# Kernel tuning notes

Hardware: AMD Instinct MI355X
Metric: run time of the kernel (lower is better)

The kernel has to match this reference:

```python
import jax, jax.numpy as jnp
import numpy as np

VOC, D, CPR, RELS = 2048, 128, 128, 7
B, DEPTH = 512, 4  # complete binary trees: 2**DEPTH leaves per tree


def setup_inputs() -> dict:
    key = jax.random.key(0)
    ks = jax.random.split(key, 13)
    s = lambda k, shape, fan: jax.random.normal(k, shape, jnp.float32) / np.sqrt(fan)
    return {
        "leaf_ids": jax.random.randint(ks[0], (B, 2, 2 ** DEPTH), 0, VOC),
        "Wv": s(ks[1], (D, VOC), VOC), "bv": jnp.zeros((D,), jnp.float32),
        "Wcps": s(ks[2], (D, 2 * D), 2 * D), "bcps": jnp.zeros((D,), jnp.float32),
        "Wcpst": s(ks[3], (D, D * D), D * D), "bcpst": jnp.zeros((D,), jnp.float32),
        "Wcpr": s(ks[4], (CPR, 2 * D), 2 * D), "bcpr": jnp.zeros((CPR,), jnp.float32),
        "Wcprt": s(ks[5], (CPR, D * D), D * D), "bcprt": jnp.zeros((CPR,), jnp.float32),
        "Wsm": s(ks[6], (RELS, CPR), CPR), "bsm": jnp.zeros((RELS,), jnp.float32),
    }


def reference(leaf_ids, Wv, bv, Wcps, bcps, Wcpst, bcpst, Wcpr, bcpr, Wcprt, bcprt, Wsm, bsm):
    d = Wv.shape[0]
    # leaf embedding: voc(one_hot(idx)) == Wv[:, idx] + bv  -> [B, 2, L, d]
    h = jnp.take(Wv.T, leaf_ids, axis=0) + bv
    # batched level-by-level tree composition (complete binary trees)
    while h.shape[2] > 1:
        l, r = h[:, :, 0::2, :], h[:, :, 1::2, :]
        lin = jnp.concatenate([l, r], axis=-1) @ Wcps.T + bcps
        kron = (l[..., :, None] * r[..., None, :]).reshape(l.shape[:-1] + (d * d,))
        h = jnp.tanh(lin + kron @ Wcpst.T + bcpst)
    lc, rc = h[:, 0, 0, :], h[:, 1, 0, :]  # [B, d] each
    cpr = jnp.concatenate([lc, rc], axis=-1) @ Wcpr.T + bcpr
    kron = (lc[:, :, None] * rc[:, None, :]).reshape(lc.shape[0], d * d)
    act = jax.nn.leaky_relu(cpr + kron @ Wcprt.T + bcprt, 0.01)
    logits = act @ Wsm.T + bsm
    return jax.nn.log_softmax(logits, axis=-1)  # [B, RELS]
```

## Files before the change

### kernel.cpp

```cpp
#include <hip/hip_runtime.h>
#include <hip/hip_bf16.h>
#include <hip/hip_fp16.h>

#define DD    128
#define VOCAB 2048
#define NRELS 7
#define NWF   (130 * 16384)

typedef _Float16 f16;
typedef __attribute__((ext_vector_type(8))) _Float16 f16x8;
typedef __attribute__((ext_vector_type(4))) float    f32x4;

__device__ __forceinline__ float lde(const void* p, size_t i, int bf) {
    if (bf) return (float)((const __hip_bfloat16*)p)[i];
    return ((const float*)p)[i];
}

__global__ void detect_kernel(const unsigned short* __restrict__ wv, int* __restrict__ flag)
{
    if (threadIdx.x == 0 && blockIdx.x == 0) {
        int sane = 0;
        for (int i = 0; i < 64; ++i) {
            unsigned e = (wv[i] >> 7) & 0xFFu;
            if (e >= 90u && e <= 160u) ++sane;
        }
        *flag = (sane == 64) ? 1 : 0;
    }
}

__global__ void prep_wvt(const void* Wv, const void* bv, const int* __restrict__ flag,
                         f16* __restrict__ WvT)
{
    const int bf = *flag;
    __shared__ float tile[64][65];
    int vt = blockIdx.x >> 1;
    int dt = blockIdx.x & 1;
    int tx = threadIdx.x & 63, ty = threadIdx.x >> 6;
    for (int yy = ty; yy < 64; yy += 4)
        tile[yy][tx] = lde(Wv, (size_t)(dt * 64 + yy) * VOCAB + vt * 64 + tx, bf);
    __syncthreads();
    for (int yy = ty; yy < 64; yy += 4) {
        int v = vt * 64 + yy, d = dt * 64 + tx;
        WvT[(size_t)v * DD + d] = (f16)(tile[tx][yy] + lde(bv, d, bf));
    }
}

__global__ void prep_wf(const void* Wcps, const void* Wcpst, const void* Wcpr, const void* Wcprt,
                        const void* bcps, const void* bcpst, const void* bcpr, const void* bcprt,
                        const void* Wsm, const void* bsm, const int* __restrict__ flag,
                        f16* __restrict__ Wext, f16* __restrict__ Wfin,
                        float* __restrict__ bias_lvl, float* __restrict__ bias_fin,
                        float* __restrict__ Wsm_f, float* __restrict__ bsm_f)
{
    const int bf = *flag;
    const int b = blockIdx.x;
    const int tid = threadIdx.x;
    if (b >= 2080) {
        if (tid < 128)      bias_lvl[tid] = lde(bcps, tid, bf) + lde(bcpst, tid, bf);
        else if (tid < 256) bias_fin[tid - 128] = lde(bcpr, tid - 128, bf) + lde(bcprt, tid - 128, bf);
        for (int o = tid; o < NRELS * DD; o += 256) Wsm_f[o] = lde(Wsm, o, bf);
        if (tid < NRELS) bsm_f[tid] = lde(bsm, tid, bf);
        return;
    }
    const int which = b / 1040;
    const int rem   = b - which * 1040;
    const int i     = rem >> 3;
    const int n8    = rem & 7;
    const void* Wt = which ? (const void*)Wcprt : (const void*)Wcpst;
    const void* Ws = which ? (const void*)Wcpr  : (const void*)Wcps;
    f16* dst = which ? Wfin : Wext;

    __shared__ float tile[16 * 129];
    #pragma unroll
    for (int it = 0; it < 8; ++it) {
        int idx = it * 256 + tid;
        int rr = idx >> 7, c = idx & 127;
        float v = (i < 128) ? lde(Wt, (size_t)(n8 * 16 + rr) * 16384 + (size_t)i * 128 + c, bf)
                            : lde(Ws, (size_t)(n8 * 16 + rr) * 256 + (size_t)(i - 128) * 128 + c, bf);
        tile[rr * 129 + c] = v;
    }
    __syncthreads();
    f16* out = dst + (size_t)(i * 8 + n8) * 2048;
    #pragma unroll
    for (int it = 0; it < 8; ++it) {
        int o = it * 256 + tid;
        int t = o >> 9, ln = (o >> 3) & 63, e = o & 7;
        out[o] = (f16)tile[(ln & 15) * 129 + t * 32 + ((ln >> 4) << 3) + e];
    }
}

__global__ void embed_kernel(const int* __restrict__ ids,
                             const f16* __restrict__ WvT, f16* __restrict__ h0)
{
    int t = blockIdx.x * 256 + threadIdx.x;
    int row = t >> 4;
    int c = (t & 15) * 8;
    int id = ids[row];
    *(f16x8*)&h0[(size_t)row * DD + c] = *(const f16x8*)&WvT[(size_t)id * DD + c];
}

__launch_bounds__(128, 2)
__global__ void gemm_kernel(const f16* __restrict__ hin, const f16* __restrict__ Wf,
                            f16* __restrict__ part, int Mrows, int S, int BI)
{
    __shared__ f16 Lt[128 * 128];

    const int tid  = threadIdx.x;
    const int lane = tid & 63;
    const int wv   = tid >> 6;
    const int b    = blockIdx.x;
    const int nh   = (b >> 2) & 1;
    const int r    = ((b >> 3) << 2) | (b & 3);
    const int mb   = r / S;
    const int s    = r - mb * S;
    const int m0   = mb * 128;
    const int i0   = s * BI;
    const int nI   = BI + ((s == 1 || s == 2) ? 1 : 0);
    const int NSt  = nI * 4;

    #pragma unroll
    for (int it = 0; it < 16; ++it) {
        int c  = it * 128 + tid;
        int mm = c >> 4;
        int cb = c & 15;
        f16x8 v = *(const f16x8*)&hin[(size_t)(2 * (m0 + mm)) * DD + cb * 8];
        *(f16x8*)&Lt[mm * 128 + ((cb ^ (mm & 15)) << 3)] = v;
    }

    const int mrow = lane & 15;
    const int q    = lane >> 4;
    const int wm   = wv * 64;

    f16x8 rf[4][4];
    #pragma unroll
    for (int mt = 0; mt < 4; ++mt)
        #pragma unroll
        for (int t = 0; t < 4; ++t)
            rf[mt][t] = *(const f16x8*)&hin[(size_t)(2 * (m0 + wm + mt * 16 + mrow) + 1) * DD + t * 32 + q * 8];

    __syncthreads();

    auto imap = [&](int ii) { return (ii < BI) ? (i0 + ii) : (s == 1 ? 128 : 129); };
    const f16* wb0 = Wf + nh * 8192 + lane * 8;
    auto ldW = [&](int st, f16x8* d) {
        int i = imap(st >> 2), t = st & 3;
        const f16* p = wb0 + (size_t)i * 16384 + t * 512;
        #pragma unroll
        for (int nt = 0; nt < 4; ++nt) d[nt] = *(const f16x8*)(p + nt * 2048);
    };
    auto lpRead = [&](int i, int mt) -> f16 {
        return Lt[(wm + mt * 16 + mrow) * 128 + (((i >> 3) ^ mrow) << 3) + (i & 7)];
    };

    f32x4 acc[4][4] = {};
    f16x8 wbuf[2][4];
    f16 lpv[4], lpn[4];

    ldW(0, wbuf[0]);
    {
        int i = imap(0);
        if (i < 128) {
            #pragma unroll
            for (int mt = 0; mt < 4; ++mt) lpv[mt] = lpRead(i, mt);
        }
    }

    for (int ii = 0; ii < nI; ++ii) {
        const int i = imap(ii);
        f16x8 lb[4];
        if (i < 128) {
            #pragma unroll
            for (int mt = 0; mt < 4; ++mt) {
                f16 v = lpv[mt];
                #pragma unroll
                for (int e = 0; e < 8; ++e) lb[mt][e] = v;
            }
        }
        #pragma unroll
        for (int t = 0; t < 4; ++t) {
            const int st = ii * 4 + t;
            if (st + 1 < NSt) ldW(st + 1, wbuf[(t + 1) & 1]);
            if (t == 1 && ii + 1 < nI) {
                int i2 = imap(ii + 1);
                if (i2 < 128) {
                    #pragma unroll
                    for (int mt = 0; mt < 4; ++mt) lpn[mt] = lpRead(i2, mt);
                }
            }
            const f16x8* wc = wbuf[t & 1];
            if (i < 128) {
                #pragma unroll
                for (int mt = 0; mt < 4; ++mt) {
                    f16x8 a = lb[mt] * rf[mt][t];
                    #pragma unroll
                    for (int nt = 0; nt < 4; ++nt)
                        acc[mt][nt] = __builtin_amdgcn_mfma_f32_16x16x32_f16(a, wc[nt], acc[mt][nt], 0, 0, 0);
                }
            } else if (i == 128) {
                #pragma unroll
                for (int mt = 0; mt < 4; ++mt) {
                    f16x8 a = *(const f16x8*)&Lt[(wm + mt * 16 + mrow) * 128 + (((t * 4 + q) ^ mrow) << 3)];
                    #pragma unroll
                    for (int nt = 0; nt < 4; ++nt)
                        acc[mt][nt] = __builtin_amdgcn_mfma_f32_16x16x32_f16(a, wc[nt], acc[mt][nt], 0, 0, 0);
                }
            } else {
                #pragma unroll
                for (int mt = 0; mt < 4; ++mt) {
                    #pragma unroll
                    for (int nt = 0; nt < 4; ++nt)
                        acc[mt][nt] = __builtin_amdgcn_mfma_f32_16x16x32_f16(rf[mt][t], wc[nt], acc[mt][nt], 0, 0, 0);
                }
            }
        }
        #pragma unroll
        for (int mt = 0; mt < 4; ++mt) lpv[mt] = lpn[mt];
    }

    f16* pb = part + ((size_t)s * Mrows + m0) * DD + nh * 64;
    #pragma unroll
    for (int mt = 0; mt < 4; ++mt)
        #pragma unroll
        for (int nt = 0; nt < 4; ++nt) {
            int colg = nt * 16 + mrow;
            #pragma unroll
            for (int rr = 0; rr < 4; ++rr) {
                int rowl = wm + mt * 16 + q * 4 + rr;
                pb[(size_t)rowl * DD + colg] = (f16)acc[mt][nt][rr];
            }
        }
}

__global__ void epi_level(const f16* __restrict__ part, const float* __restrict__ bias,
                          f16* __restrict__ hout, int Mrows, int S)
{
    int idx = (blockIdx.x * 256 + threadIdx.x) * 8;
    size_t stride = (size_t)Mrows * DD;
    float sum[8] = {};
    for (int s2 = 0; s2 < S; ++s2) {
        f16x8 v = *(const f16x8*)&part[(size_t)s2 * stride + idx];
        #pragma unroll
        for (int e = 0; e < 8; ++e) sum[e] += (float)v[e];
    }
    int n = idx & 127;
    f16x8 o;
    #pragma unroll
    for (int e = 0; e < 8; ++e) o[e] = (f16)tanhf(sum[e] + bias[n + e]);
    *(f16x8*)&hout[idx] = o;
}

__global__ void fin_epi(const f16* __restrict__ part, const float* __restrict__ bias,
                        const float* __restrict__ Wsm_f, const float* __restrict__ bsm_f,
                        const int* __restrict__ flag, void* __restrict__ outp, int S)
{
    int lane = threadIdx.x & 63;
    int wv = threadIdx.x >> 6;
    int p = blockIdx.x * 4 + wv;
    size_t stride = (size_t)512 * DD;
    const f16* base = part + (size_t)p * DD;
    float a0 = 0.f, a1 = 0.f;
    for (int s2 = 0; s2 < S; ++s2) {
        a0 += (float)base[(size_t)s2 * stride + lane];
        a1 += (float)base[(size_t)s2 * stride + 64 + lane];
    }
    a0 += bias[lane];      a1 += bias[64 + lane];
    a0 = (a0 > 0.f) ? a0 : 0.01f * a0;
    a1 = (a1 > 0.f) ? a1 : 0.01f * a1;
    float lg[NRELS];
    #pragma unroll
    for (int r = 0; r < NRELS; ++r) {
        float pr = a0 * Wsm_f[r * DD + lane] + a1 * Wsm_f[r * DD + 64 + lane];
        #pragma unroll
        for (int d = 1; d < 64; d <<= 1) pr += __shfl_xor(pr, d, 64);
        lg[r] = pr + bsm_f[r];
    }
    float mx = lg[0];
    #pragma unroll
    for (int r = 1; r < NRELS; ++r) mx = fmaxf(mx, lg[r]);
    float se = 0.f;
    #pragma unroll
    for (int r = 0; r < NRELS; ++r) se += expf(lg[r] - mx);
    float lse = logf(se) + mx;
    if (lane < NRELS) {
        float v = lg[lane] - lse;
        if (*flag) ((__hip_bfloat16*)outp)[p * NRELS + lane] = __float2bfloat16(v);
        else       ((float*)outp)[p * NRELS + lane] = v;
    }
}

extern "C" void kernel_launch(void* const* d_in, const int* in_sizes, int n_in,
                              void* d_out, int out_size, void* d_ws, size_t ws_size,
                              hipStream_t stream)
{
    const int* ids = (const int*)d_in[0];

    char* ws = (char*)d_ws;
    f16*   part     = (f16*)ws;
    f16*   h0       = (f16*)(ws + ((size_t)16 << 20));
    f16*   h1       = (f16*)(ws + ((size_t)20 << 20));
    f16*   h2       = (f16*)(ws + ((size_t)22 << 20));
    f16*   h3       = (f16*)(ws + ((size_t)23 << 20));
    f16*   h4       = (f16*)(ws + ((size_t)23 << 20) + (512 << 10));
    f16*   WvT      = (f16*)(ws + ((size_t)24 << 20));
    f16*   Wext     = (f16*)(ws + ((size_t)24 << 20) + (512 << 10));
    f16*   Wfin     = Wext + (size_t)NWF;
    float* bias_lvl = (float*)(Wfin + (size_t)NWF);
    float* bias_fin = bias_lvl + 128;
    int*   flag     = (int*)(bias_fin + 128);
    float* Wsm_f    = (float*)(flag + 16);
    float* bsm_f    = Wsm_f + NRELS * DD;

    if (ws_size < ((size_t)34 << 20)) return;

    detect_kernel<<<1, 64, 0, stream>>>((const unsigned short*)d_in[1], flag);
    prep_wvt<<<64, 256, 0, stream>>>(d_in[1], d_in[2], flag, WvT);
    prep_wf<<<2081, 256, 0, stream>>>(d_in[3], d_in[5], d_in[7], d_in[9],
                                      d_in[4], d_in[6], d_in[8], d_in[10],
                                      d_in[11], d_in[12], flag,
                                      Wext, Wfin, bias_lvl, bias_fin, Wsm_f, bsm_f);
    embed_kernel<<<1024, 256, 0, stream>>>(ids, WvT, h0);

    gemm_kernel<<<1024, 128, 0, stream>>>(h0, Wext, part, 8192, 8, 16);
    epi_level<<<512, 256, 0, stream>>>(part, bias_lvl, h1, 8192, 8);
    gemm_kernel<<<1024, 128, 0, stream>>>(h1, Wext, part, 4096, 16, 8);
    epi_level<<<256, 256, 0, stream>>>(part, bias_lvl, h2, 4096, 16);
    gemm_kernel<<<1024, 128, 0, stream>>>(h2, Wext, part, 2048, 32, 4);
    epi_level<<<128, 256, 0, stream>>>(part, bias_lvl, h3, 2048, 32);
    gemm_kernel<<<1024, 128, 0, stream>>>(h3, Wext, part, 1024, 64, 2);
    epi_level<<<64, 256, 0, stream>>>(part, bias_lvl, h4, 1024, 64);
    gemm_kernel<<<1024, 128, 0, stream>>>(h4, Wfin, part, 512, 128, 1);
    fin_epi<<<128, 256, 0, stream>>>(part, bias_fin, Wsm_f, bsm_f, flag, d_out, 128);
}
```

Baseline: 311.0 us.

## Fuse prep and embed kernels, deepen weight prefetch, rebalance late-level split-K

Merges the dtype-detect, WvT transpose and weight-packing kernels into a single prep launch, with each block recomputing the bf16 detection inline. The embedding gather is folded into the first GEMM by indexing WvT through the leaf ids, so the h0 buffer and the embed kernel go away. The GEMM weight prefetch moves from double to quadruple buffering, issuing loads a few steps ahead. The last two levels use fewer split-K slices and half the blocks, which shrinks the partial-sum traffic at the cost of less parallelism and more register pressure from the larger buffer.

After: 343.1 us. +10.3%, slower.

```diff
diff --git a/kernel.cpp b/kernel.cpp
--- a/kernel.cpp
+++ b/kernel.cpp
@@ -16,54 +16,53 @@
     return ((const float*)p)[i];
 }
 
-__global__ void detect_kernel(const unsigned short* __restrict__ wv, int* __restrict__ flag)
-{
-    if (threadIdx.x == 0 && blockIdx.x == 0) {
-        int sane = 0;
-        for (int i = 0; i < 64; ++i) {
-            unsigned e = (wv[i] >> 7) & 0xFFu;
-            if (e >= 90u && e <= 160u) ++sane;
-        }
-        *flag = (sane == 64) ? 1 : 0;
-    }
-}
-
-__global__ void prep_wvt(const void* Wv, const void* bv, const int* __restrict__ flag,
-                         f16* __restrict__ WvT)
-{
-    const int bf = *flag;
-    __shared__ float tile[64][65];
-    int vt = blockIdx.x >> 1;
-    int dt = blockIdx.x & 1;
-    int tx = threadIdx.x & 63, ty = threadIdx.x >> 6;
-    for (int yy = ty; yy < 64; yy += 4)
-        tile[yy][tx] = lde(Wv, (size_t)(dt * 64 + yy) * VOCAB + vt * 64 + tx, bf);
-    __syncthreads();
-    for (int yy = ty; yy < 64; yy += 4) {
-        int v = vt * 64 + yy, d = dt * 64 + tx;
-        WvT[(size_t)v * DD + d] = (f16)(tile[tx][yy] + lde(bv, d, bf));
-    }
-}
-
-__global__ void prep_wf(const void* Wcps, const void* Wcpst, const void* Wcpr, const void* Wcprt,
-                        const void* bcps, const void* bcpst, const void* bcpr, const void* bcprt,
-                        const void* Wsm, const void* bsm, const int* __restrict__ flag,
-                        f16* __restrict__ Wext, f16* __restrict__ Wfin,
-                        float* __restrict__ bias_lvl, float* __restrict__ bias_fin,
-                        float* __restrict__ Wsm_f, float* __restrict__ bsm_f)
-{
-    const int bf = *flag;
+__device__ __forceinline__ int detect_bf(const unsigned short* wv) {
+    int sane = 0;
+    #pragma unroll
+    for (int i = 0; i < 64; ++i) {
+        unsigned e = (wv[i] >> 7) & 0xFFu;
+        sane += (e >= 90u && e <= 160u) ? 1 : 0;
+    }
+    return sane == 64;
+}
+
+__global__ void prep_all(const void* Wv, const void* bv,
+                         const void* Wcps, const void* bcps,
+                         const void* Wcpst, const void* bcpst,
+                         const void* Wcpr, const void* bcpr,
+                         const void* Wcprt, const void* bcprt,
+                         const void* Wsm, const void* bsm,
+                         f16* __restrict__ WvT, f16* __restrict__ Wext, f16* __restrict__ Wfin,
+                         float* __restrict__ bias_lvl, float* __restrict__ bias_fin,
+                         float* __restrict__ Wsm_f, float* __restrict__ bsm_f)
+{
+    const int bf = detect_bf((const unsigned short*)Wv);
     const int b = blockIdx.x;
     const int tid = threadIdx.x;
-    if (b >= 2080) {
+
+    if (b < 64) {
+        __shared__ float tile[64][65];
+        int vt = b >> 1, dt = b & 1;
+        int tx = tid & 63, ty = tid >> 6;
+        for (int yy = ty; yy < 64; yy += 4)
+            tile[yy][tx] = lde(Wv, (size_t)(dt * 64 + yy) * VOCAB + vt * 64 + tx, bf);
+        __syncthreads();
+        for (int yy = ty; yy < 64; yy += 4) {
+            int v = vt * 64 + yy, d = dt * 64 + tx;
+            WvT[(size_t)v * DD + d] = (f16)(tile[tx][yy] + lde(bv, d, bf));
+        }
+        return;
+    }
+    if (b >= 2144) {
         if (tid < 128)      bias_lvl[tid] = lde(bcps, tid, bf) + lde(bcpst, tid, bf);
         else if (tid < 256) bias_fin[tid - 128] = lde(bcpr, tid - 128, bf) + lde(bcprt, tid - 128, bf);
         for (int o = tid; o < NRELS * DD; o += 256) Wsm_f[o] = lde(Wsm, o, bf);
         if (tid < NRELS) bsm_f[tid] = lde(bsm, tid, bf);
         return;
     }
-    const int which = b / 1040;
-    const int rem   = b - which * 1040;
+    const int bb    = b - 64;
+    const int which = bb / 1040;
+    const int rem   = bb - which * 1040;
     const int i     = rem >> 3;
     const int n8    = rem & 7;
     const void* Wt = which ? (const void*)Wcprt : (const void*)Wcpst;
@@ -89,18 +88,9 @@
     }
 }
 
-__global__ void embed_kernel(const int* __restrict__ ids,
-                             const f16* __restrict__ WvT, f16* __restrict__ h0)
-{
-    int t = blockIdx.x * 256 + threadIdx.x;
-    int row = t >> 4;
-    int c = (t & 15) * 8;
-    int id = ids[row];
-    *(f16x8*)&h0[(size_t)row * DD + c] = *(const f16x8*)&WvT[(size_t)id * DD + c];
-}
-
 __launch_bounds__(128, 2)
-__global__ void gemm_kernel(const f16* __restrict__ hin, const f16* __restrict__ Wf,
+__global__ void gemm_kernel(const f16* __restrict__ hin, const int* __restrict__ ids,
+                            const f16* __restrict__ Wf,
                             f16* __restrict__ part, int Mrows, int S, int BI)
 {
     __shared__ f16 Lt[128 * 128];
@@ -123,7 +113,8 @@
         int c  = it * 128 + tid;
         int mm = c >> 4;
         int cb = c & 15;
-        f16x8 v = *(const f16x8*)&hin[(size_t)(2 * (m0 + mm)) * DD + cb * 8];
+        int row = ids ? ids[2 * (m0 + mm)] : 2 * (m0 + mm);
+        f16x8 v = *(const f16x8*)&hin[(size_t)row * DD + cb * 8];
         *(f16x8*)&Lt[mm * 128 + ((cb ^ (mm & 15)) << 3)] = v;
     }
 
@@ -133,18 +124,20 @@
 
     f16x8 rf[4][4];
     #pragma unroll
-    for (int mt = 0; mt < 4; ++mt)
+    for (int mt = 0; mt < 4; ++mt) {
+        int p = m0 + wm + mt * 16 + mrow;
+        int row = ids ? ids[2 * p + 1] : 2 * p + 1;
         #pragma unroll
         for (int t = 0; t < 4; ++t)
-            rf[mt][t] = *(const f16x8*)&hin[(size_t)(2 * (m0 + wm + mt * 16 + mrow) + 1) * DD + t * 32 + q * 8];
+            rf[mt][t] = *(const f16x8*)&hin[(size_t)row * DD + t * 32 + q * 8];
+    }
 
     __syncthreads();
 
     auto imap = [&](int ii) { return (ii < BI) ? (i0 + ii) : (s == 1 ? 128 : 129); };
     const f16* wb0 = Wf + nh * 8192 + lane * 8;
-    auto ldW = [&](int st, f16x8* d) {
-        int i = imap(st >> 2), t = st & 3;
-        const f16* p = wb0 + (size_t)i * 16384 + t * 512;
+    auto ldW = [&](int ic, int tt, f16x8* d) {
+        const f16* p = wb0 + (size_t)imap(ic) * 16384 + tt * 512;
         #pragma unroll
         for (int nt = 0; nt < 4; ++nt) d[nt] = *(const f16x8*)(p + nt * 2048);
     };
@@ -153,10 +146,12 @@
     };
 
     f32x4 acc[4][4] = {};
-    f16x8 wbuf[2][4];
+    f16x8 wbuf[4][4];
     f16 lpv[4], lpn[4];
 
-    ldW(0, wbuf[0]);
+    ldW(0, 0, wbuf[0]);
+    ldW(0, 1, wbuf[1]);
+    ldW(0, 2, wbuf[2]);
     {
         int i = imap(0);
         if (i < 128) {
@@ -165,8 +160,36 @@
         }
     }
 
+#define TSTEP(T) {                                                                      \
+    const f16x8* wc = wbuf[T];                                                          \
+    if (i < 128) {                                                                      \
+        _Pragma("unroll")                                                               \
+        for (int mt = 0; mt < 4; ++mt) {                                                \
+            f16x8 a = lb[mt] * rf[mt][T];                                               \
+            _Pragma("unroll")                                                           \
+            for (int nt = 0; nt < 4; ++nt)                                              \
+                acc[mt][nt] = __builtin_amdgcn_mfma_f32_16x16x32_f16(a, wc[nt], acc[mt][nt], 0, 0, 0); \
+        }                                                                               \
+    } else if (i == 128) {                                                              \
+        _Pragma("unroll")                                                               \
+        for (int mt = 0; mt < 4; ++mt) {                                                \
+            f16x8 a = *(const f16x8*)&Lt[(wm + mt * 16 + mrow) * 128 + ((((T) * 4 + q) ^ mrow) << 3)]; \
+            _Pragma("unroll")                                                           \
+            for (int nt = 0; nt < 4; ++nt)                                              \
+                acc[mt][nt] = __builtin_amdgcn_mfma_f32_16x16x32_f16(a, wc[nt], acc[mt][nt], 0, 0, 0); \
+        }                                                                               \
+    } else {                                                                            \
+        _Pragma("unroll")                                                               \
+        for (int mt = 0; mt < 4; ++mt) {                                                \
+            _Pragma("unroll")                                                           \
+            for (int nt = 0; nt < 4; ++nt)                                              \
+                acc[mt][nt] = __builtin_amdgcn_mfma_f32_16x16x32_f16(rf[mt][T], wc[nt], acc[mt][nt], 0, 0, 0); \
+        }                                                                               \
+    } }
+
     for (int ii = 0; ii < nI; ++ii) {
         const int i = imap(ii);
+        const bool more = (ii + 1 < nI);
         f16x8 lb[4];
         if (i < 128) {
             #pragma unroll
@@ -176,46 +199,25 @@
                 for (int e = 0; e < 8; ++e) lb[mt][e] = v;
             }
         }
-        #pragma unroll
-        for (int t = 0; t < 4; ++t) {
-            const int st = ii * 4 + t;
-            if (st + 1 < NSt) ldW(st + 1, wbuf[(t + 1) & 1]);
-            if (t == 1 && ii + 1 < nI) {
-                int i2 = imap(ii + 1);
-                if (i2 < 128) {
-                    #pragma unroll
-                    for (int mt = 0; mt < 4; ++mt) lpn[mt] = lpRead(i2, mt);
-                }
+        ldW(ii, 3, wbuf[3]);
+        TSTEP(0);
+        if (more) {
+            ldW(ii + 1, 0, wbuf[0]);
+            int i2 = imap(ii + 1);
+            if (i2 < 128) {
+                #pragma unroll
+                for (int mt = 0; mt < 4; ++mt) lpn[mt] = lpRead(i2, mt);
             }
-            const f16x8* wc = wbuf[t & 1];
-            if (i < 128) {
-                #pragma unroll
-                for (int mt = 0; mt < 4; ++mt) {
-                    f16x8 a = lb[mt] * rf[mt][t];
-                    #pragma unroll
-                    for (int nt = 0; nt < 4; ++nt)
-                        acc[mt][nt] = __builtin_amdgcn_mfma_f32_16x16x32_f16(a, wc[nt], acc[mt][nt], 0, 0, 0);
-                }
-            } else if (i == 128) {
-                #pragma unroll
-                for (int mt = 0; mt < 4; ++mt) {
-                    f16x8 a = *(const f16x8*)&Lt[(wm + mt * 16 + mrow) * 128 + (((t * 4 + q) ^ mrow) << 3)];
-                    #pragma unroll
-                    for (int nt = 0; nt < 4; ++nt)
-                        acc[mt][nt] = __builtin_amdgcn_mfma_f32_16x16x32_f16(a, wc[nt], acc[mt][nt], 0, 0, 0);
-                }
-            } else {
-                #pragma unroll
-                for (int mt = 0; mt < 4; ++mt) {
-                    #pragma unroll
-                    for (int nt = 0; nt < 4; ++nt)
-                        acc[mt][nt] = __builtin_amdgcn_mfma_f32_16x16x32_f16(rf[mt][t], wc[nt], acc[mt][nt], 0, 0, 0);
-                }
-            }
-        }
+        }
+        TSTEP(1);
+        if (more) ldW(ii + 1, 1, wbuf[1]);
+        TSTEP(2);
+        if (more) ldW(ii + 1, 2, wbuf[2]);
+        TSTEP(3);
         #pragma unroll
         for (int mt = 0; mt < 4; ++mt) lpv[mt] = lpn[mt];
     }
+#undef TSTEP
 
     f16* pb = part + ((size_t)s * Mrows + m0) * DD + nh * 64;
     #pragma unroll
@@ -251,7 +253,7 @@
 
 __global__ void fin_epi(const f16* __restrict__ part, const float* __restrict__ bias,
                         const float* __restrict__ Wsm_f, const float* __restrict__ bsm_f,
-                        const int* __restrict__ flag, void* __restrict__ outp, int S)
+                        const unsigned short* __restrict__ wv_raw, void* __restrict__ outp, int S)
 {
     int lane = threadIdx.x & 63;
     int wv = threadIdx.x >> 6;
@@ -283,8 +285,8 @@
     float lse = logf(se) + mx;
     if (lane < NRELS) {
         float v = lg[lane] - lse;
-        if (*flag) ((__hip_bfloat16*)outp)[p * NRELS + lane] = __float2bfloat16(v);
-        else       ((float*)outp)[p * NRELS + lane] = v;
+        if (detect_bf(wv_raw)) ((__hip_bfloat16*)outp)[p * NRELS + lane] = __float2bfloat16(v);
+        else                   ((float*)outp)[p * NRELS + lane] = v;
     }
 }
 
@@ -296,7 +298,6 @@
 
     char* ws = (char*)d_ws;
     f16*   part     = (f16*)ws;
-    f16*   h0       = (f16*)(ws + ((size_t)16 << 20));
     f16*   h1       = (f16*)(ws + ((size_t)20 << 20));
     f16*   h2       = (f16*)(ws + ((size_t)22 << 20));
     f16*   h3       = (f16*)(ws + ((size_t)23 << 20));
@@ -306,28 +307,24 @@
     f16*   Wfin     = Wext + (size_t)NWF;
     float* bias_lvl = (float*)(Wfin + (size_t)NWF);
     float* bias_fin = bias_lvl + 128;
-    int*   flag     = (int*)(bias_fin + 128);
-    float* Wsm_f    = (float*)(flag + 16);
+    float* Wsm_f    = bias_fin + 128;
     float* bsm_f    = Wsm_f + NRELS * DD;
 
     if (ws_size < ((size_t)34 << 20)) return;
 
-    detect_kernel<<<1, 64, 0, stream>>>((const unsigned short*)d_in[1], flag);
-    prep_wvt<<<64, 256, 0, stream>>>(d_in[1], d_in[2], flag, WvT);
-    prep_wf<<<2081, 256, 0, stream>>>(d_in[3], d_in[5], d_in[7], d_in[9],
-                                      d_in[4], d_in[6], d_in[8], d_in[10],
-                                      d_in[11], d_in[12], flag,
-                                      Wext, Wfin, bias_lvl, bias_fin, Wsm_f, bsm_f);
-    embed_kernel<<<1024, 256, 0, stream>>>(ids, WvT, h0);
-
-    gemm_kernel<<<1024, 128, 0, stream>>>(h0, Wext, part, 8192, 8, 16);
+    prep_all<<<2145, 256, 0, stream>>>(d_in[1], d_in[2], d_in[3], d_in[4], d_in[5], d_in[6],
+                                       d_in[7], d_in[8], d_in[9], d_in[10], d_in[11], d_in[12],
+                                       WvT, Wext, Wfin, bias_lvl, bias_fin, Wsm_f, bsm_f);
+
+    gemm_kernel<<<1024, 128, 0, stream>>>(WvT, ids, Wext, part, 8192, 8, 16);
     epi_level<<<512, 256, 0, stream>>>(part, bias_lvl, h1, 8192, 8);
-    gemm_kernel<<<1024, 128, 0, stream>>>(h1, Wext, part, 4096, 16, 8);
+    gemm_kernel<<<1024, 128, 0, stream>>>(h1, nullptr, Wext, part, 4096, 16, 8);
     epi_level<<<256, 256, 0, stream>>>(part, bias_lvl, h2, 4096, 16);
-    gemm_kernel<<<1024, 128, 0, stream>>>(h2, Wext, part, 2048, 32, 4);
+    gemm_kernel<<<1024, 128, 0, stream>>>(h2, nullptr, Wext, part, 2048, 32, 4);
     epi_level<<<128, 256, 0, stream>>>(part, bias_lvl, h3, 2048, 32);
-    gemm_kernel<<<1024, 128, 0, stream>>>(h3, Wext, part, 1024, 64, 2);
-    epi_level<<<64, 256, 0, stream>>>(part, bias_lvl, h4, 1024, 64);
-    gemm_kernel<<<1024, 128, 0, stream>>>(h4, Wfin, part, 512, 128, 1);
-    fin_epi<<<128, 256, 0, stream>>>(part, bias_fin, Wsm_f, bsm_f, flag, d_out, 128);
-}
+    gemm_kernel<<<512, 128, 0, stream>>>(h3, nullptr, Wext, part, 1024, 32, 4);
+    epi_level<<<64, 256, 0, stream>>>(part, bias_lvl, h4, 1024, 32);
+    gemm_kernel<<<512, 128, 0, stream>>>(h4, nullptr, Wfin, part, 512, 64, 2);
+    fin_epi<<<128, 256, 0, stream>>>(part, bias_fin, Wsm_f, bsm_f,
+                                     (const unsigned short*)d_in[1], d_out, 64);
+}
```
